# Kernel optimization log

Hardware: AMD Instinct MI355X
Metric: run time of the kernel (lower is better)

## Reference

```python
import jax, jax.numpy as jnp
import numpy as np

B, S, D = 2, 2048, 1024
H, HD = 16, 64
MAX_OFF = 64
FC_LAYERS = 4


def _rope_tables(seq_len, head_dim):
    inv_freq = 1.0 / (10000.0 ** (jnp.arange(0, head_dim, 2, dtype=jnp.float32) / head_dim))
    t = jnp.arange(seq_len, dtype=jnp.float32)
    freqs = jnp.einsum('s,d->sd', t, inv_freq)
    emb = jnp.concatenate([freqs, freqs], axis=-1)  # [S, HD]
    return jnp.cos(emb), jnp.sin(emb)


def _rotate_half(x):
    h = x.shape[-1] // 2
    return jnp.concatenate([-x[..., h:], x[..., :h]], axis=-1)


def _fc_mask(bar_ids, instrument_ids):
    # rule tables indexed by clamped bar offset (key_bar - query_bar) + MAX_OFF
    same_rules = jnp.zeros(2 * MAX_OFF + 1, dtype=bool).at[MAX_OFF:].set(True)
    cross_rules = (jnp.zeros(2 * MAX_OFF + 1, dtype=bool)
                   .at[MAX_OFF:MAX_OFF + 3].set(True)
                   .at[MAX_OFF + 4].set(True))
    off = jnp.clip(bar_ids[:, None, :] - bar_ids[:, :, None], -MAX_OFF, MAX_OFF) + MAX_OFF  # [B,S,S]
    k_real = instrument_ids[:, None, :] < 129
    q_real = instrument_ids[:, :, None] < 129
    same = (instrument_ids[:, None, :] == instrument_ids[:, :, None]) & k_real & q_real
    diff = (~same) & k_real & q_real
    mask = (same & same_rules[off]) | (diff & cross_rules[off])
    # global key tokens (instrument 129 or bar -1) visible to every query
    is_global_k = (instrument_ids[:, None, :] == 129) | (bar_ids[:, None, :] == -1)  # [B,1,S]
    mask = mask | is_global_k
    s = bar_ids.shape[1]
    causal = jnp.tril(jnp.ones((s, s), dtype=bool))
    return mask & causal[None]  # [B,S,S]


def setup_inputs() -> dict:
    key = jax.random.key(0)
    ks = jax.random.split(key, 12)
    sc = 1.0 / np.sqrt(D)
    return {
        'x': jax.random.normal(ks[0], (B, S, D), jnp.float32),
        'bar_ids': jnp.sort(jax.random.randint(ks[1], (B, S), 0, 128), axis=-1),
        'instrument_ids': jax.random.randint(ks[2], (B, S), 0, 130),
        'layer_idx': 0,
        'Wq': jax.random.normal(ks[3], (D, D), jnp.float32) * sc,
        'bq': jnp.zeros((D,), jnp.float32),
        'Wk': jax.random.normal(ks[4], (D, D), jnp.float32) * sc,
        'bk': jnp.zeros((D,), jnp.float32),
        'Wv': jax.random.normal(ks[5], (D, D), jnp.float32) * sc,
        'bv': jnp.zeros((D,), jnp.float32),
        'Wo': jax.random.normal(ks[6], (D, D), jnp.float32) * sc,
        'bo': jnp.zeros((D,), jnp.float32),
    }


def reference(x, bar_ids, instrument_ids, layer_idx, Wq, bq, Wk, bk, Wv, bv, Wo, bo):
    b, s, d = x.shape
    q = (x @ Wq + bq).reshape(b, s, H, HD).transpose(0, 2, 1, 3)  # [B,H,S,HD]
    k = (x @ Wk + bk).reshape(b, s, H, HD).transpose(0, 2, 1, 3)
    v = (x @ Wv + bv).reshape(b, s, H, HD).transpose(0, 2, 1, 3)
    cos, sin = _rope_tables(s, HD)  # [S,HD], broadcasts over [B,H,S,HD]
    q = q * cos + _rotate_half(q) * sin
    k = k * cos + _rotate_half(k) * sin
    if layer_idx < FC_LAYERS:
        mask = _fc_mask(bar_ids, instrument_ids)  # [B,S,S]
    else:
        mask = jnp.broadcast_to(jnp.tril(jnp.ones((s, s), dtype=bool)), (b, s, s))
    bias = jnp.where(mask[:, None, :, :], 0.0, -jnp.inf).astype(x.dtype)
    scores = jnp.einsum('bhqd,bhkd->bhqk', q, k) * (HD ** -0.5) + bias
    attn = jax.nn.softmax(scores, axis=-1)
    out = jnp.einsum('bhqk,bhkd->bhqd', attn, v)
    out = out.transpose(0, 2, 1, 3).reshape(b, s, d)
    return out @ Wo + bo
```

## Files before the change

### kernel.cpp

```cpp
#include <hip/hip_runtime.h>
#include <hip/hip_bf16.h>

typedef unsigned short u16;
typedef unsigned u32;
typedef unsigned long long u64;
typedef float f32x4 __attribute__((ext_vector_type(4)));
typedef __bf16 bf16x8 __attribute__((ext_vector_type(8)));

#define NB 2
#define NS 2048
#define ND 1024
#define NH 16
#define HD 64

__device__ inline u16 bfbits(float f) { __bf16 h = (__bf16)f; return __builtin_bit_cast(u16, h); }

__device__ inline void gl16(const u16* g, u16* l) {
  __builtin_amdgcn_global_load_lds((const __attribute__((address_space(1))) void*)(g),
                                   (__attribute__((address_space(3))) void*)(l), 16, 0, 0);
}

__global__ void __launch_bounds__(256)
prep_all(const float* __restrict__ W0, const float* __restrict__ W1,
         const float* __restrict__ W2, const float* __restrict__ W3,
         u16* __restrict__ T0, u16* __restrict__ T1, u16* __restrict__ T2, u16* __restrict__ T3,
         const float* __restrict__ x, u16* __restrict__ xb,
         float* __restrict__ cost, float* __restrict__ sint) {
  const int bid = blockIdx.x, t = threadIdx.x;
  if (bid < 4096) {
    __shared__ float tile[32][33];
    const float* Ws[4] = {W0, W1, W2, W3};
    u16* Ts[4] = {T0, T1, T2, T3};
    const float* __restrict__ W = Ws[bid >> 10];
    u16* __restrict__ WT = Ts[bid >> 10];
    const int rem = bid & 1023;
    const int n0 = (rem & 31) * 32, k0 = (rem >> 5) * 32;
    const int tx = t & 31, ty = t >> 5;
#pragma unroll
    for (int i = 0; i < 4; ++i)
      tile[ty + i * 8][tx] = W[(size_t)(k0 + ty + i * 8) * ND + n0 + tx];
    __syncthreads();
#pragma unroll
    for (int i = 0; i < 4; ++i)
      WT[(size_t)(n0 + ty + i * 8) * ND + k0 + tx] = bfbits(tile[tx][ty + i * 8]);
  } else if (bid < 8192) {
    const int i = (bid - 4096) * 256 + t;
    float4 v = reinterpret_cast<const float4*>(x)[i];
    uint2 pk;
    pk.x = (unsigned)bfbits(v.x) | ((unsigned)bfbits(v.y) << 16);
    pk.y = (unsigned)bfbits(v.z) | ((unsigned)bfbits(v.w) << 16);
    reinterpret_cast<uint2*>(xb)[i] = pk;
  } else {
    const int i = (bid - 8192) * 256 + t;
    const int s = i >> 5, d = i & 31;
    float invf = powf(10000.f, -(float)d / 32.f);
    float a = (float)s * invf;
    cost[i] = cosf(a);
    sint[i] = sinf(a);
  }
}

__global__ void __launch_bounds__(512, 2)
gemm_qkv(const u16* __restrict__ A, const u16* __restrict__ BT3,
         const float* __restrict__ bq, const float* __restrict__ bk, const float* __restrict__ bv,
         u16* __restrict__ qbuf, u16* __restrict__ kbuf, u16* __restrict__ vtbuf,
         const float* __restrict__ cost, const float* __restrict__ sint,
         const int* __restrict__ bar, const int* __restrict__ inst,
         const int* __restrict__ lidx, u64* __restrict__ mb, u32* __restrict__ tilebits) {
  constexpr int K = ND;
  __shared__ alignas(16) u16 Alds[2][256][64];
  __shared__ alignas(16) u16 Blds[2][256][64];
  const int t = threadIdx.x;
  const int hid = (int)blockIdx.x;

  if (hid >= 192) {
    int* sbar = reinterpret_cast<int*>(&Alds[0][0][0]);
    int* sinst = sbar + NB * NS;
    int* firsts = reinterpret_cast<int*>(&Blds[0][0][0]);
    int* lasts = firsts + NB * 128;
    u64* Gw = reinterpret_cast<u64*>(lasts + NB * 128);
    for (int i = t; i < NB * NS; i += 512) {
      sbar[i] = bar[i];
      sinst[i] = inst[i];
    }
    __syncthreads();
    for (int i = t; i < NB * NS; i += 512) {
      const int idx = i & (NS - 1);
      const int v = sbar[i];
      if (v >= 0 && v < 128) {
        if (idx == 0 || sbar[i - 1] != v) firsts[(i >> 11) * 128 + v] = idx;
        if (idx == NS - 1 || sbar[i + 1] != v) lasts[(i >> 11) * 128 + v] = idx;
      }
    }
    {
      const int w8 = t >> 6, lane = t & 63;
#pragma unroll
      for (int p8 = 0; p8 < 8; ++p8) {
        const int p = w8 * 8 + p8;
        const int gb = p >> 5, gkt = p & 31;
        const int k = gkt * 64 + lane;
        const bool gbit = (sinst[gb * NS + k] == 129) || (sbar[gb * NS + k] == -1);
        const u64 wd = __ballot(gbit);
        if (lane == 0) Gw[p] = wd;
      }
    }
    __syncthreads();
    const bool fc = (lidx[0] < 4);
    const int w8 = t >> 6, lane = t & 63;
    const int gw = (hid - 192) * 8 + w8;
#pragma unroll
    for (int rr = 0; rr < 8; ++rr) {
      const int pair = gw + 512 * rr;
      const int b = pair >> 11, q = pair & (NS - 1);
      const int qt = q >> 6;
      const int qb = sbar[b * NS + q];
      const bool qreal = sinst[b * NS + q] < 129;
      int lo = NS, hi = -1;
      if (fc && qreal && qb >= 0 && qb < 128) {
        lo = firsts[b * 128 + qb];
        hi = lasts[b * 128 + qb];
      }
      const int kt = lane;
      if (kt <= qt) {
        u64 word;
        if (!fc) {
          word = ~0ULL;
        } else {
          word = Gw[b * 32 + kt];
          const int base = kt * 64;
          const int s = lo - base, e = hi - base;
          if (e >= 0 && s <= 63) {
            const int cs = s < 0 ? 0 : s;
            const int ce = e > 63 ? 63 : e;
            u64 m = (ce >= 63) ? ~0ULL : ((1ULL << (ce + 1)) - 1);
            if (cs > 0) m &= ~((1ULL << cs) - 1);
            word |= m;
          }
        }
        if (kt == qt) {
          const int qq = q & 63;
          word &= (qq >= 63) ? ~0ULL : ((1ULL << (qq + 1)) - 1);
        }
        mb[(((size_t)b * NS + q) << 5) + kt] = word;
      }
    }
    if (hid == 192 && w8 == 0) {
      const int b = lane >> 5, qt = lane & 31;
      u32 tbw;
      if (!fc) {
        tbw = (qt >= 31) ? 0xFFFFFFFFu : ((1u << (qt + 1)) - 1);
      } else {
        const int v0 = sbar[b * NS + qt * 64];
        const int v1 = sbar[b * NS + qt * 64 + 63];
        const int lo_t = (v0 >= 0 && v0 < 128) ? firsts[b * 128 + v0] : 0;
        const int hi_t = (v1 >= 0 && v1 < 128) ? lasts[b * 128 + v1] : NS - 1;
        tbw = 0;
        for (int kt = 0; kt <= qt; ++kt) {
          const bool on = (kt == qt) || (Gw[b * 32 + kt] != 0ULL) ||
                          (kt * 64 <= hi_t && kt * 64 + 63 >= lo_t);
          if (on) tbw |= (1u << kt);
        }
      }
      if (lane < 64) tilebits[lane] = tbw;
    }
    return;
  }

  const int xcd = hid & 7, j = hid >> 3;
  const int m0 = (xcd * 2 + j / 12) << 8;
  const int nblk = j % 12;
  const int proj = nblk >> 2;
  const int n0 = (nblk & 3) << 8;
  const int w = t >> 6, lane = t & 63, lr = lane & 15, lg = lane >> 4;
  const int wm = w >> 2, wn = w & 3;
  const float* __restrict__ bias = proj == 0 ? bq : (proj == 1 ? bk : bv);
  f32x4 acc[8][4] = {};

  const int srow = lane >> 3;
  const int lcol = (lane & 7) ^ srow;
  const u16* Ag = A + (size_t)(m0 + w * 32 + srow) * K + lcol * 8;
  const u16* Bg = BT3 + (size_t)(proj * ND + n0 + w * 32 + srow) * K + lcol * 8;
  const int swz = lr & 7;

#pragma unroll
  for (int c = 0; c < 4; ++c) {
    gl16(Ag + (size_t)c * 8 * K, &Alds[0][w * 32 + c * 8][0]);
    gl16(Bg + (size_t)c * 8 * K, &Blds[0][w * 32 + c * 8][0]);
  }

  for (int s = 0; s < K / 64; ++s) {
    asm volatile("s_waitcnt vmcnt(0)" ::: "memory");
    __builtin_amdgcn_s_barrier();
    if (s + 1 < K / 64) {
      const int k0n = (s + 1) * 64;
#pragma unroll
      for (int c = 0; c < 4; ++c) {
        gl16(Ag + k0n + (size_t)c * 8 * K, &Alds[(s + 1) & 1][w * 32 + c * 8][0]);
        gl16(Bg + k0n + (size_t)c * 8 * K, &Blds[(s + 1) & 1][w * 32 + c * 8][0]);
      }
    }
    const int cur = s & 1;
    bf16x8 bfr[4][2];
#pragma unroll
    for (int ni = 0; ni < 4; ++ni)
#pragma unroll
      for (int ks = 0; ks < 2; ++ks)
        bfr[ni][ks] = *reinterpret_cast<const bf16x8*>(
            &Blds[cur][wn * 64 + ni * 16 + lr][(((ks << 2) + lg) ^ swz) << 3]);
#pragma unroll
    for (int mi = 0; mi < 8; ++mi) {
#pragma unroll
      for (int ks = 0; ks < 2; ++ks) {
        const bf16x8 af = *reinterpret_cast<const bf16x8*>(
            &Alds[cur][wm * 128 + mi * 16 + lr][(((ks << 2) + lg) ^ swz) << 3]);
#pragma unroll
        for (int ni = 0; ni < 4; ++ni)
          acc[mi][ni] = __builtin_amdgcn_mfma_f32_16x16x32_bf16(af, bfr[ni][ks], acc[mi][ni], 0, 0, 0);
      }
    }
  }

  if (proj < 2) {
    u16* out = proj ? kbuf : qbuf;
    const float qs = proj == 0 ? 0.18033688f : 1.0f;
    const int colbase = n0 + wn * 64;
    const int h = colbase >> 6;
#pragma unroll
    for (int mi = 0; mi < 8; ++mi)
#pragma unroll
      for (int r = 0; r < 4; ++r) {
        const int row = m0 + wm * 128 + mi * 16 + lg * 4 + r;
        const int b = row >> 11, s = row & (NS - 1);
        u16* op = out + ((size_t)(b * NH + h) * NS + s) * HD;
#pragma unroll
        for (int nf = 0; nf < 2; ++nf) {
          const int dlo = nf * 16 + lr;
          float lo = acc[mi][nf][r] + bias[colbase + dlo];
          float hi = acc[mi][nf + 2][r] + bias[colbase + dlo + 32];
          float c = cost[s * 32 + dlo], si = sint[s * 32 + dlo];
          const u32 pk = (u32)bfbits((lo * c - hi * si) * qs) |
                         ((u32)bfbits((hi * c + lo * si) * qs) << 16);
          *reinterpret_cast<u32*>(op + 2 * dlo) = pk;
        }
      }
  } else {
    u16* out = vtbuf;
#pragma unroll
    for (int mi = 0; mi < 8; ++mi)
#pragma unroll
      for (int ni = 0; ni < 4; ++ni) {
        const int col = n0 + wn * 64 + ni * 16 + lr;
        const int h = col >> 6, d = col & 63;
        const int s0 = m0 + wm * 128 + mi * 16 + lg * 4;
        const int b = s0 >> 11, s = s0 & (NS - 1);
        uint2 pk;
        pk.x = (unsigned)bfbits(acc[mi][ni][0] + bias[col]) |
               ((unsigned)bfbits(acc[mi][ni][1] + bias[col]) << 16);
        pk.y = (unsigned)bfbits(acc[mi][ni][2] + bias[col]) |
               ((unsigned)bfbits(acc[mi][ni][3] + bias[col]) << 16);
        *reinterpret_cast<uint2*>(out + ((size_t)(b * NH + h) * HD + d) * NS + s) = pk;
      }
  }
}

__global__ void __launch_bounds__(512)
gemm_out(const u16* __restrict__ A, const u16* __restrict__ BT, const float* __restrict__ bias,
         float* __restrict__ out) {
  constexpr int K = ND;
  __shared__ alignas(16) u16 Alds[3][128][64];
  __shared__ alignas(16) u16 Blds[3][128][64];
  const int t = threadIdx.x;
  const int hid = (int)blockIdx.x;
  const int n0 = (hid & 7) * 128;
  const int m0 = (hid >> 3) * 128;
  const int w = t >> 6, lane = t & 63, lr = lane & 15, lg = lane >> 4;
  const int wm = w >> 1, wn = w & 1;
  f32x4 acc[2][4] = {};

  const int srow = lane >> 3;
  const int lcol = (lane & 7) ^ srow;
  const u16* Ag = A + (size_t)(m0 + w * 16 + srow) * K + lcol * 8;
  const u16* Bg = BT + (size_t)(n0 + w * 16 + srow) * K + lcol * 8;
  const int swz = lr & 7;

#pragma unroll
  for (int p = 0; p < 2; ++p) {
#pragma unroll
    for (int c = 0; c < 2; ++c) {
      gl16(Ag + p * 64 + (size_t)c * 8 * K, &Alds[p][w * 16 + c * 8][0]);
      gl16(Bg + p * 64 + (size_t)c * 8 * K, &Blds[p][w * 16 + c * 8][0]);
    }
  }

  int cur = 0;
  for (int s = 0; s < K / 64; ++s) {
    if (s + 1 < K / 64) {
      asm volatile("s_waitcnt vmcnt(4)" ::: "memory");
    } else {
      asm volatile("s_waitcnt vmcnt(0)" ::: "memory");
    }
    __builtin_amdgcn_s_barrier();
    if (s + 2 < K / 64) {
      int bn = cur + 2;
      if (bn >= 3) bn -= 3;
      const int k0n = (s + 2) * 64;
#pragma unroll
      for (int c = 0; c < 2; ++c) {
        gl16(Ag + k0n + (size_t)c * 8 * K, &Alds[bn][w * 16 + c * 8][0]);
        gl16(Bg + k0n + (size_t)c * 8 * K, &Blds[bn][w * 16 + c * 8][0]);
      }
    }
    bf16x8 bfr[4][2];
#pragma unroll
    for (int ni = 0; ni < 4; ++ni)
#pragma unroll
      for (int ks = 0; ks < 2; ++ks)
        bfr[ni][ks] = *reinterpret_cast<const bf16x8*>(
            &Blds[cur][wn * 64 + ni * 16 + lr][(((ks << 2) + lg) ^ swz) << 3]);
#pragma unroll
    for (int mi = 0; mi < 2; ++mi) {
#pragma unroll
      for (int ks = 0; ks < 2; ++ks) {
        const bf16x8 af = *reinterpret_cast<const bf16x8*>(
            &Alds[cur][wm * 32 + mi * 16 + lr][(((ks << 2) + lg) ^ swz) << 3]);
#pragma unroll
        for (int ni = 0; ni < 4; ++ni)
          acc[mi][ni] = __builtin_amdgcn_mfma_f32_16x16x32_bf16(af, bfr[ni][ks], acc[mi][ni], 0, 0, 0);
      }
    }
    cur = (cur == 2) ? 0 : cur + 1;
  }

#pragma unroll
  for (int mi = 0; mi < 2; ++mi)
#pragma unroll
    for (int r = 0; r < 4; ++r) {
      const int row = m0 + wm * 32 + mi * 16 + lg * 4 + r;
#pragma unroll
      for (int ni = 0; ni < 4; ++ni) {
        const int col = n0 + wn * 64 + ni * 16 + lr;
        out[(size_t)row * ND + col] = acc[mi][ni][r] + bias[col];
      }
    }
}

__global__ void __launch_bounds__(256, 4)
attn_fused(const u16* __restrict__ qb, const u16* __restrict__ kb, const u16* __restrict__ vtb,
           const u64* __restrict__ mb, const u32* __restrict__ tilebits,
           u16* __restrict__ attnout) {
  __shared__ alignas(16) u16 Klds[2][64][64];
  __shared__ alignas(16) u16 Vlds[2][64][64];
  __shared__ alignas(16) u16 Plds[4][16][64];
  const int t = threadIdx.x, w = t >> 6, lane = t & 63, lr = lane & 15, lg = lane >> 4;
  const int hid = (int)blockIdx.x;
  const int xcd = hid & 7, ix = hid >> 3;
  const int g = ix >> 5, r0 = ix & 31;
  const int bh = xcd * 4 + (r0 >> 3);
  const int b = bh >> 4, h = bh & 15;
  const int j = r0 & 7;
  const int qt = (g == 0) ? 31 - j : (g == 1) ? j : (g == 2) ? 23 - j : 8 + j;
  const int qbase = qt * 64;
  const u16* __restrict__ qh = qb + (size_t)(b * NH + h) * NS * HD;
  const u16* __restrict__ kh = kb + (size_t)(b * NH + h) * NS * HD;
  const u16* __restrict__ vth = vtb + (size_t)(b * NH + h) * HD * NS;
  const u32 bits = tilebits[b * 32 + qt];
  const int nt = __popc(bits);

  const int srow = lane >> 3;
  const int lcol = (lane & 7) ^ srow;
  const int sw = lr & 7;

  const int qrow = qbase + w * 16 + lr;
  const bf16x8 qf0 = *reinterpret_cast<const bf16x8*>(qh + (size_t)qrow * HD + lg * 8);
  const bf16x8 qf1 = *reinterpret_cast<const bf16x8*>(qh + (size_t)qrow * HD + 32 + lg * 8);
  const u64* __restrict__ mrow = mb + (((size_t)b * NS + qrow) << 5);

  float m_s = -1e30f, l_s = 0.f;
  f32x4 oacc[4] = {};
  int cur = 0;

  const int kt0 = __ffs(bits) - 1;
  u32 rem = bits & (bits - 1);
  {
    const int kb0 = kt0 << 6;
#pragma unroll
    for (int c = 0; c < 2; ++c) {
      const int row = w * 16 + c * 8 + srow;
      gl16(kh + (size_t)(kb0 + row) * HD + lcol * 8, &Klds[0][w * 16 + c * 8][0]);
      gl16(vth + (size_t)row * NS + kb0 + lcol * 8, &Vlds[0][w * 16 + c * 8][0]);
    }
  }
  u64 mw = mrow[kt0];

  for (int i = 0; i < nt; ++i) {
    __syncthreads();
    u64 mwn = 0ULL;
    if (rem) {
      const int ktn = __ffs(rem) - 1;
      rem &= rem - 1;
      const int kb0n = ktn << 6;
#pragma unroll
      for (int c = 0; c < 2; ++c) {
        const int row = w * 16 + c * 8 + srow;
        gl16(kh + (size_t)(kb0n + row) * HD + lcol * 8, &Klds[cur ^ 1][w * 16 + c * 8][0]);
        gl16(vth + (size_t)row * NS + kb0n + lcol * 8, &Vlds[cur ^ 1][w * 16 + c * 8][0]);
      }
      mwn = mrow[ktn];
    }

    if (!__all(mw == 0ULL)) {
      const u16* Kb = &Klds[cur][0][0];
      const u16* Vb = &Vlds[cur][0][0];

      f32x4 sacc[4] = {};
      __builtin_amdgcn_s_setprio(1);
#pragma unroll
      for (int n = 0; n < 4; ++n) {
        const u16* kr = Kb + (n * 16 + lr) * 64;
        bf16x8 kf0 = *reinterpret_cast<const bf16x8*>(kr + ((lg ^ sw) << 3));
        bf16x8 kf1 = *reinterpret_cast<const bf16x8*>(kr + (((4 + lg) ^ sw) << 3));
        sacc[n] = __builtin_amdgcn_mfma_f32_16x16x32_bf16(kf0, qf0, sacc[n], 0, 0, 0);
        sacc[n] = __builtin_amdgcn_mfma_f32_16x16x32_bf16(kf1, qf1, sacc[n], 0, 0, 0);
      }
      __builtin_amdgcn_s_setprio(0);

      float pm[4][4];
      float mx4[4];
#pragma unroll
      for (int n = 0; n < 4; ++n) {
#pragma unroll
        for (int r = 0; r < 4; ++r) {
          const bool vis = (mw >> (n * 16 + lg * 4 + r)) & 1ULL;
          pm[n][r] = vis ? sacc[n][r] : -3e30f;
        }
        mx4[n] = fmaxf(fmaxf(pm[n][0], pm[n][1]), fmaxf(pm[n][2], pm[n][3]));
      }
      float mx = fmaxf(fmaxf(mx4[0], mx4[1]), fmaxf(mx4[2], mx4[3]));
      mx = fmaxf(mx, __shfl_xor(mx, 16));
      mx = fmaxf(mx, __shfl_xor(mx, 32));

      const bool skip = __all(mx <= m_s + 11.5415603f);
      const float mn = skip ? m_s : fmaxf(m_s, mx);

      float rs = 0.f;
#pragma unroll
      for (int n = 0; n < 4; ++n) {
        const float e0 = exp2f(pm[n][0] - mn);
        const float e1 = exp2f(pm[n][1] - mn);
        const float e2 = exp2f(pm[n][2] - mn);
        const float e3 = exp2f(pm[n][3] - mn);
        rs += (e0 + e1) + (e2 + e3);
        uint2 pk;
        pk.x = (unsigned)bfbits(e0) | ((unsigned)bfbits(e1) << 16);
        pk.y = (unsigned)bfbits(e2) | ((unsigned)bfbits(e3) << 16);
        *reinterpret_cast<uint2*>(&Plds[w][lr][(((n << 2) + lg) ^ (lr & 14)) << 2]) = pk;
      }
      rs += __shfl_xor(rs, 16);
      rs += __shfl_xor(rs, 32);

      if (skip) {
        l_s += rs;
      } else {
        const float sf = exp2f(m_s - mn);
        m_s = mn;
        l_s = l_s * sf + rs;
        float sfr[4];
#pragma unroll
        for (int r = 0; r < 4; ++r) sfr[r] = __shfl(sf, lg * 4 + r);
#pragma unroll
        for (int nd = 0; nd < 4; ++nd)
#pragma unroll
          for (int r = 0; r < 4; ++r) oacc[nd][r] *= sfr[r];
      }

      const bf16x8 pf0 = *reinterpret_cast<const bf16x8*>(&Plds[w][lr][((2 * lg) ^ (lr & 14)) << 2]);
      const bf16x8 pf1 = *reinterpret_cast<const bf16x8*>(&Plds[w][lr][((8 + 2 * lg) ^ (lr & 14)) << 2]);
      __builtin_amdgcn_s_setprio(1);
#pragma unroll
      for (int nd = 0; nd < 4; ++nd) {
        const u16* vr = Vb + (nd * 16 + lr) * 64;
        bf16x8 vf0 = *reinterpret_cast<const bf16x8*>(vr + ((lg ^ sw) << 3));
        bf16x8 vf1 = *reinterpret_cast<const bf16x8*>(vr + (((4 + lg) ^ sw) << 3));
        oacc[nd] = __builtin_amdgcn_mfma_f32_16x16x32_bf16(pf0, vf0, oacc[nd], 0, 0, 0);
        oacc[nd] = __builtin_amdgcn_mfma_f32_16x16x32_bf16(pf1, vf1, oacc[nd], 0, 0, 0);
      }
      __builtin_amdgcn_s_setprio(0);
    }

    mw = mwn;
    cur ^= 1;
  }

  float il[4];
#pragma unroll
  for (int r = 0; r < 4; ++r) il[r] = 1.f / __shfl(l_s, lg * 4 + r);
#pragma unroll
  for (int nd = 0; nd < 4; ++nd)
#pragma unroll
    for (int r = 0; r < 4; ++r) {
      const int i = qbase + w * 16 + lg * 4 + r;
      attnout[(size_t)(b * NS + i) * ND + h * HD + nd * 16 + lr] = bfbits(oacc[nd][r] * il[r]);
    }
}

extern "C" void kernel_launch(void* const* d_in, const int* in_sizes, int n_in,
                              void* d_out, int out_size, void* d_ws, size_t ws_size,
                              hipStream_t stream) {
  const float* x = (const float*)d_in[0];
  const int* bar = (const int*)d_in[1];
  const int* inst = (const int*)d_in[2];
  const int* lidx = (const int*)d_in[3];
  const float* Wq = (const float*)d_in[4];
  const float* bq = (const float*)d_in[5];
  const float* Wk = (const float*)d_in[6];
  const float* bk = (const float*)d_in[7];
  const float* Wv = (const float*)d_in[8];
  const float* bv = (const float*)d_in[9];
  const float* Wo = (const float*)d_in[10];
  const float* bo = (const float*)d_in[11];
  float* out = (float*)d_out;

  char* ws = (char*)d_ws;
  constexpr size_t XB = (size_t)NB * NS * ND * 2;
  constexpr size_t WT = (size_t)ND * ND * 2;
  u16* xb   = (u16*)(ws);
  u16* WqT  = (u16*)(ws + XB);
  u16* WkT  = (u16*)(ws + XB + 1 * WT);
  u16* WvT  = (u16*)(ws + XB + 2 * WT);
  u16* WoT  = (u16*)(ws + XB + 3 * WT);
  u16* qbuf = (u16*)(ws + XB + 4 * WT);
  u16* kbuf = (u16*)(ws + XB + 4 * WT + XB);
  u16* vtbuf= (u16*)(ws + XB + 4 * WT + 2 * XB);
  float* cost = (float*)(ws + XB + 4 * WT + 3 * XB);
  float* sint = cost + NS * 32;
  u64* maskbuf = (u64*)(ws + XB + 4 * WT + 3 * XB + (size_t)NS * 32 * 4 * 2);
  u32* tilebits = (u32*)((char*)maskbuf + (size_t)NB * NS * 32 * 8);
  u16* attnout = xb;

  prep_all<<<dim3(8448), 256, 0, stream>>>(Wq, Wk, Wv, Wo, WqT, WkT, WvT, WoT,
                                           x, xb, cost, sint);

  gemm_qkv<<<dim3(256), 512, 0, stream>>>(xb, WqT, bq, bk, bv, qbuf, kbuf, vtbuf, cost, sint,
                                          bar, inst, lidx, maskbuf, tilebits);

  attn_fused<<<dim3(1024), 256, 0, stream>>>(qbuf, kbuf, vtbuf, maskbuf, tilebits, attnout);

  gemm_out<<<dim3(256), 512, 0, stream>>>(attnout, WoT, bo, out);
}
```

Before: 110.4 us.

## Halve QKV GEMM M-tile and add three-stage LDS prefetch pipeline

Shrinks the QKV projection tile from 256x256 to 128x256, doubling GEMM workgroups from 192 to 384 to fill more of the device's compute units. It also moves from double to triple buffering, issuing loads two k-steps ahead with a partial vmcnt wait so memory latency overlaps with MFMA work. The trade-off is lower arithmetic intensity per tile, more total global/L2 traffic for the B operand, and a different LDS footprint that may affect occupancy. Mask-building blocks are shifted to start at index 384, with their scratch pointers remapped onto the resized shared buffers.

```diff
diff --git a/kernel.cpp b/kernel.cpp
--- a/kernel.cpp
+++ b/kernel.cpp
@@ -68,15 +68,16 @@
          const int* __restrict__ bar, const int* __restrict__ inst,
          const int* __restrict__ lidx, u64* __restrict__ mb, u32* __restrict__ tilebits) {
   constexpr int K = ND;
-  __shared__ alignas(16) u16 Alds[2][256][64];
-  __shared__ alignas(16) u16 Blds[2][256][64];
+  constexpr int NT = K / 64;
+  __shared__ alignas(16) u16 Alds[3][128][64];
+  __shared__ alignas(16) u16 Blds[3][256][64];
   const int t = threadIdx.x;
   const int hid = (int)blockIdx.x;
 
-  if (hid >= 192) {
-    int* sbar = reinterpret_cast<int*>(&Alds[0][0][0]);
+  if (hid >= 384) {
+    int* sbar = reinterpret_cast<int*>(&Blds[0][0][0]);
     int* sinst = sbar + NB * NS;
-    int* firsts = reinterpret_cast<int*>(&Blds[0][0][0]);
+    int* firsts = reinterpret_cast<int*>(&Alds[0][0][0]);
     int* lasts = firsts + NB * 128;
     u64* Gw = reinterpret_cast<u64*>(lasts + NB * 128);
     for (int i = t; i < NB * NS; i += 512) {
@@ -107,7 +108,7 @@
     __syncthreads();
     const bool fc = (lidx[0] < 4);
     const int w8 = t >> 6, lane = t & 63;
-    const int gw = (hid - 192) * 8 + w8;
+    const int gw = (hid - 384) * 8 + w8;
 #pragma unroll
     for (int rr = 0; rr < 8; ++rr) {
       const int pair = gw + 512 * rr;
@@ -144,7 +145,7 @@
         mb[(((size_t)b * NS + q) << 5) + kt] = word;
       }
     }
-    if (hid == 192 && w8 == 0) {
+    if (hid == 384 && w8 == 0) {
       const int b = lane >> 5, qt = lane & 31;
       u32 tbw;
       if (!fc) {
@@ -167,39 +168,50 @@
   }
 
   const int xcd = hid & 7, j = hid >> 3;
-  const int m0 = (xcd * 2 + j / 12) << 8;
+  const int m0 = (xcd * 4 + j / 12) << 7;
   const int nblk = j % 12;
   const int proj = nblk >> 2;
   const int n0 = (nblk & 3) << 8;
   const int w = t >> 6, lane = t & 63, lr = lane & 15, lg = lane >> 4;
   const int wm = w >> 2, wn = w & 3;
   const float* __restrict__ bias = proj == 0 ? bq : (proj == 1 ? bk : bv);
-  f32x4 acc[8][4] = {};
+  f32x4 acc[4][4] = {};
 
   const int srow = lane >> 3;
   const int lcol = (lane & 7) ^ srow;
-  const u16* Ag = A + (size_t)(m0 + w * 32 + srow) * K + lcol * 8;
+  const u16* Ag = A + (size_t)(m0 + w * 16 + srow) * K + lcol * 8;
   const u16* Bg = BT3 + (size_t)(proj * ND + n0 + w * 32 + srow) * K + lcol * 8;
   const int swz = lr & 7;
 
 #pragma unroll
-  for (int c = 0; c < 4; ++c) {
-    gl16(Ag + (size_t)c * 8 * K, &Alds[0][w * 32 + c * 8][0]);
-    gl16(Bg + (size_t)c * 8 * K, &Blds[0][w * 32 + c * 8][0]);
-  }
-
-  for (int s = 0; s < K / 64; ++s) {
-    asm volatile("s_waitcnt vmcnt(0)" ::: "memory");
+  for (int p = 0; p < 2; ++p) {
+#pragma unroll
+    for (int c = 0; c < 2; ++c)
+      gl16(Ag + p * 64 + (size_t)c * 8 * K, &Alds[p][w * 16 + c * 8][0]);
+#pragma unroll
+    for (int c = 0; c < 4; ++c)
+      gl16(Bg + p * 64 + (size_t)c * 8 * K, &Blds[p][w * 32 + c * 8][0]);
+  }
+
+  int cur = 0;
+  for (int s = 0; s < NT; ++s) {
+    if (s + 1 < NT) {
+      asm volatile("s_waitcnt vmcnt(6)" ::: "memory");
+    } else {
+      asm volatile("s_waitcnt vmcnt(0)" ::: "memory");
+    }
     __builtin_amdgcn_s_barrier();
-    if (s + 1 < K / 64) {
-      const int k0n = (s + 1) * 64;
-#pragma unroll
-      for (int c = 0; c < 4; ++c) {
-        gl16(Ag + k0n + (size_t)c * 8 * K, &Alds[(s + 1) & 1][w * 32 + c * 8][0]);
-        gl16(Bg + k0n + (size_t)c * 8 * K, &Blds[(s + 1) & 1][w * 32 + c * 8][0]);
-      }
-    }
-    const int cur = s & 1;
+    if (s + 2 < NT) {
+      int bn = cur + 2;
+      if (bn >= 3) bn -= 3;
+      const int k0n = (s + 2) * 64;
+#pragma unroll
+      for (int c = 0; c < 2; ++c)
+        gl16(Ag + k0n + (size_t)c * 8 * K, &Alds[bn][w * 16 + c * 8][0]);
+#pragma unroll
+      for (int c = 0; c < 4; ++c)
+        gl16(Bg + k0n + (size_t)c * 8 * K, &Blds[bn][w * 32 + c * 8][0]);
+    }
     bf16x8 bfr[4][2];
 #pragma unroll
     for (int ni = 0; ni < 4; ++ni)
@@ -208,16 +220,17 @@
         bfr[ni][ks] = *reinterpret_cast<const bf16x8*>(
             &Blds[cur][wn * 64 + ni * 16 + lr][(((ks << 2) + lg) ^ swz) << 3]);
 #pragma unroll
-    for (int mi = 0; mi < 8; ++mi) {
+    for (int mi = 0; mi < 4; ++mi) {
 #pragma unroll
       for (int ks = 0; ks < 2; ++ks) {
         const bf16x8 af = *reinterpret_cast<const bf16x8*>(
-            &Alds[cur][wm * 128 + mi * 16 + lr][(((ks << 2) + lg) ^ swz) << 3]);
+            &Alds[cur][wm * 64 + mi * 16 + lr][(((ks << 2) + lg) ^ swz) << 3]);
 #pragma unroll
         for (int ni = 0; ni < 4; ++ni)
           acc[mi][ni] = __builtin_amdgcn_mfma_f32_16x16x32_bf16(af, bfr[ni][ks], acc[mi][ni], 0, 0, 0);
       }
     }
+    cur = (cur == 2) ? 0 : cur + 1;
   }
 
   if (proj < 2) {
@@ -226,10 +239,10 @@
     const int colbase = n0 + wn * 64;
     const int h = colbase >> 6;
 #pragma unroll
-    for (int mi = 0; mi < 8; ++mi)
+    for (int mi = 0; mi < 4; ++mi)
 #pragma unroll
       for (int r = 0; r < 4; ++r) {
-        const int row = m0 + wm * 128 + mi * 16 + lg * 4 + r;
+        const int row = m0 + wm * 64 + mi * 16 + lg * 4 + r;
         const int b = row >> 11, s = row & (NS - 1);
         u16* op = out + ((size_t)(b * NH + h) * NS + s) * HD;
 #pragma unroll
@@ -246,12 +259,12 @@
   } else {
     u16* out = vtbuf;
 #pragma unroll
-    for (int mi = 0; mi < 8; ++mi)
+    for (int mi = 0; mi < 4; ++mi)
 #pragma unroll
       for (int ni = 0; ni < 4; ++ni) {
         const int col = n0 + wn * 64 + ni * 16 + lr;
         const int h = col >> 6, d = col & 63;
-        const int s0 = m0 + wm * 128 + mi * 16 + lg * 4;
+        const int s0 = m0 + wm * 64 + mi * 16 + lg * 4;
         const int b = s0 >> 11, s = s0 & (NS - 1);
         uint2 pk;
         pk.x = (unsigned)bfbits(acc[mi][ni][0] + bias[col]) |
@@ -540,7 +553,7 @@
   prep_all<<<dim3(8448), 256, 0, stream>>>(Wq, Wk, Wv, Wo, WqT, WkT, WvT, WoT,
                                            x, xb, cost, sint);
 
-  gemm_qkv<<<dim3(256), 512, 0, stream>>>(xb, WqT, bq, bk, bv, qbuf, kbuf, vtbuf, cost, sint,
+  gemm_qkv<<<dim3(448), 512, 0, stream>>>(xb, WqT, bq, bk, bv, qbuf, kbuf, vtbuf, cost, sint,
                                           bar, inst, lidx, maskbuf, tilebits);
 
   attn_fused<<<dim3(1024), 256, 0, stream>>>(qbuf, kbuf, vtbuf, maskbuf, tilebits, attnout);
```

Measured after the change: 113.0 us. 1.02x slower.
